# Optimization experiments

Measured on AMD Instinct MI355X. Metric: run time of the kernel, lower is better.

## Reference

```python
import jax, jax.numpy as jnp
import numpy as np
import math

N_EMBED = 2048
N_HEAD = 16
HEAD_DIM = N_EMBED // N_HEAD  # 128
ROPE_BASE = 10000.0


def _rope_tables(T, dim, dtype):
    # inv_freq over even indices, emb = concat(freqs, freqs) along last dim
    inv_freq = 1.0 / (ROPE_BASE ** (jnp.arange(0, dim, 2, dtype=jnp.float32) / dim))
    t = jnp.arange(T, dtype=jnp.float32)
    freqs = jnp.einsum('i,j->ij', t, inv_freq)          # [T, dim/2]
    emb = jnp.concatenate([freqs, freqs], axis=-1)      # [T, dim]
    return jnp.cos(emb).astype(dtype), jnp.sin(emb).astype(dtype)


def _rotate_half(x):
    h = x.shape[-1] // 2
    return jnp.concatenate([-x[..., h:], x[..., :h]], axis=-1)


def setup_inputs() -> dict:
    key = jax.random.key(0)
    ks = jax.random.split(key, 5)
    B, T, C = 32, 256, N_EMBED
    s = 1.0 / math.sqrt(C)
    return {
        'x': jax.random.normal(ks[0], (B, T, C), dtype=jnp.float32),
        'wq': jax.random.normal(ks[1], (C, C), dtype=jnp.float32) * s,
        'wk': jax.random.normal(ks[2], (C, C), dtype=jnp.float32) * s,
        'wv': jax.random.normal(ks[3], (C, C), dtype=jnp.float32) * s,
        'wo': jax.random.normal(ks[4], (C, C), dtype=jnp.float32) * s,
    }


def reference(x, wq, wk, wv, wo):
    B, T, C = x.shape
    H, D = N_HEAD, HEAD_DIM
    # torch Linear: y = x @ W^T
    q = (x @ wq.T).reshape(B, T, H, D).transpose(0, 2, 1, 3)  # [B,H,T,D]
    k = (x @ wk.T).reshape(B, T, H, D).transpose(0, 2, 1, 3)
    v = (x @ wv.T).reshape(B, T, H, D).transpose(0, 2, 1, 3)

    cos, sin = _rope_tables(T, D, x.dtype)  # [T,D] each, broadcast over B,H
    q = q * cos + _rotate_half(q) * sin
    k = k * cos + _rotate_half(k) * sin

    att = jnp.einsum('bhqd,bhkd->bhqk', q, k) / math.sqrt(D)
    causal = jnp.triu(jnp.ones((T, T), dtype=bool), k=1)
    att = jnp.where(causal, jnp.finfo(att.dtype).min, att)
    att = jax.nn.softmax(att, axis=-1)
    # dropout p=0.0 -> identity
    y = jnp.einsum('bhqk,bhkd->bhqd', att, v)
    y = y.transpose(0, 2, 1, 3).reshape(B, T, C)
    return y @ wo.T
```

## Files before the change

kernel.cpp:

```cpp
#include <hip/hip_runtime.h>

#define HB 32
#define HT 256
#define HC 2048
#define HH 16
#define HD 128
#define HM (HB * HT)

typedef __bf16 bf16x8 __attribute__((ext_vector_type(8)));
typedef float f32x4 __attribute__((ext_vector_type(4)));
typedef float f32x16 __attribute__((ext_vector_type(16)));

__device__ __forceinline__ unsigned short f2bf(float f) {
  unsigned u = __float_as_uint(f);
  u += 0x7FFFu + ((u >> 16) & 1u);
  return (unsigned short)(u >> 16);
}
__device__ __forceinline__ float bf2f(unsigned short h) {
  return __uint_as_float(((unsigned)h) << 16);
}

__global__ __launch_bounds__(256) void cvt_all(
    const float* __restrict__ x, const float* __restrict__ wq, const float* __restrict__ wk,
    const float* __restrict__ wv, const float* __restrict__ wo,
    unsigned short* __restrict__ xb, unsigned short* __restrict__ wqb,
    unsigned short* __restrict__ wkb, unsigned short* __restrict__ wvb,
    unsigned short* __restrict__ wob) {
  size_t i = (size_t)blockIdx.x * 256 + threadIdx.x;
  const float* src;
  unsigned short* dst;
  size_t off;
  if (i < 4194304) {
    src = x; dst = xb; off = i;
  } else {
    size_t j = i - 4194304;
    int w = (int)(j >> 20);
    off = j & 1048575;
    src = (w == 0) ? wq : (w == 1) ? wk : (w == 2) ? wv : wo;
    dst = (w == 0) ? wqb : (w == 1) ? wkb : (w == 2) ? wvb : wob;
  }
  float4 v = ((const float4*)src)[off];
  ushort4 o;
  o.x = f2bf(v.x); o.y = f2bf(v.y); o.z = f2bf(v.z); o.w = f2bf(v.w);
  ((ushort4*)dst)[off] = o;
}

__device__ __forceinline__ void gl_lds16(const unsigned short* g, unsigned short* l) {
  __builtin_amdgcn_global_load_lds((const __attribute__((address_space(1))) void*)g,
                                   (__attribute__((address_space(3))) void*)l, 16, 0, 0);
}

__device__ __forceinline__ void gemm_core32(const unsigned short* __restrict__ Ab,
                                            const unsigned short* __restrict__ Wb,
                                            unsigned short* lsA, unsigned short* lsB,
                                            f32x16 acc[2][2], int tid) {
  const int lane = tid & 63, wave = tid >> 6;
  const int l31 = lane & 31, half = lane >> 5;
  const int wr = wave >> 1, wc = wave & 1;
  for (int kt = 0; kt < HC / 64; ++kt) {
    __syncthreads();
#pragma unroll
    for (int i = 0; i < 4; i++) {
      int c = i * 256 + tid;
      int row = c >> 3, cc = c & 7;
      int gc = cc ^ (row & 7);
      gl_lds16(Ab + (size_t)row * HC + kt * 64 + gc * 8, lsA + c * 8);
      gl_lds16(Wb + (size_t)row * HC + kt * 64 + gc * 8, lsB + c * 8);
    }
    __syncthreads();
#pragma unroll
    for (int ks = 0; ks < 4; ++ks) {
      const int g = ks * 2 + half;
      bf16x8 af[2], bfr[2];
#pragma unroll
      for (int mi = 0; mi < 2; mi++) {
        int r = wr * 64 + mi * 32 + l31;
        int cc = g ^ (r & 7);
        af[mi] = *(const bf16x8*)(lsA + r * 64 + cc * 8);
      }
#pragma unroll
      for (int nj = 0; nj < 2; nj++) {
        int r = nj * 64 + wc * 32 + l31;
        int cc = g ^ (r & 7);
        bfr[nj] = *(const bf16x8*)(lsB + r * 64 + cc * 8);
      }
#pragma unroll
      for (int mi = 0; mi < 2; mi++)
#pragma unroll
        for (int nj = 0; nj < 2; nj++)
          acc[mi][nj] = __builtin_amdgcn_mfma_f32_32x32x16_bf16(af[mi], bfr[nj], acc[mi][nj], 0, 0, 0);
    }
  }
}

__global__ __launch_bounds__(256) void gemm_out(const unsigned short* __restrict__ A,
                                                const unsigned short* __restrict__ W,
                                                float* __restrict__ outp) {
  __shared__ __align__(16) unsigned short lsA[128 * 64];
  __shared__ __align__(16) unsigned short lsB[128 * 64];
  const int tid = threadIdx.x;
  const int lane = tid & 63, wave = tid >> 6;
  const int l31 = lane & 31, half = lane >> 5;
  const int wr = wave >> 1, wc = wave & 1;
  const int bm = blockIdx.x, bn = blockIdx.y;

  f32x16 acc[2][2];
#pragma unroll
  for (int i = 0; i < 2; i++)
#pragma unroll
    for (int j = 0; j < 2; j++)
#pragma unroll
      for (int r = 0; r < 16; r++) acc[i][j][r] = 0.f;

  gemm_core32(A + (size_t)bm * 128 * HC, W + (size_t)bn * 128 * HC, lsA, lsB, acc, tid);

#pragma unroll
  for (int mi = 0; mi < 2; mi++)
#pragma unroll
    for (int nj = 0; nj < 2; nj++)
#pragma unroll
      for (int g = 0; g < 4; g++)
#pragma unroll
        for (int rr = 0; rr < 4; rr++) {
          int m = bm * 128 + wr * 64 + mi * 32 + rr + 8 * g + 4 * half;
          int n = bn * 128 + nj * 64 + wc * 32 + l31;
          outp[(size_t)m * HC + n] = acc[mi][nj][g * 4 + rr];
        }
}

__global__ __launch_bounds__(256) void gemm_qkv(const unsigned short* __restrict__ A,
                                                const unsigned short* __restrict__ W0,
                                                const unsigned short* __restrict__ W1,
                                                const unsigned short* __restrict__ W2,
                                                unsigned short* __restrict__ Qo,
                                                unsigned short* __restrict__ Ko,
                                                unsigned short* __restrict__ Vto) {
  __shared__ __align__(16) unsigned short lsA[128 * 64];
  __shared__ __align__(16) unsigned short lsB[128 * 64];
  const int tid = threadIdx.x;
  const int lane = tid & 63, wave = tid >> 6;
  const int l31 = lane & 31, half = lane >> 5;
  const int wr = wave >> 1, wc = wave & 1;
  const int bm = blockIdx.x;
  const int which = blockIdx.y >> 4;
  const int bn = blockIdx.y & 15;

  f32x16 acc[2][2];
#pragma unroll
  for (int i = 0; i < 2; i++)
#pragma unroll
    for (int j = 0; j < 2; j++)
#pragma unroll
      for (int r = 0; r < 16; r++) acc[i][j][r] = 0.f;

  if (which < 2) {
    const unsigned short* W = (which == 0) ? W0 : W1;
    unsigned short* outp = (which == 0) ? Qo : Ko;
    gemm_core32(A + (size_t)bm * 128 * HC, W + (size_t)bn * 128 * HC, lsA, lsB, acc, tid);
    const int dlo = wc * 32 + l31;
    const float invf = __expf((float)dlo * (-0.14391156831212787f));
    const int h = bn;
#pragma unroll
    for (int mi = 0; mi < 2; mi++)
#pragma unroll
      for (int g = 0; g < 4; g++)
#pragma unroll
        for (int rr = 0; rr < 4; rr++) {
          int m = bm * 128 + wr * 64 + mi * 32 + rr + 8 * g + 4 * half;
          int t = m & 255, b = m >> 8;
          float ang = (float)t * invf;
          float sn, cs;
          __sincosf(ang, &sn, &cs);
          int reg = g * 4 + rr;
          float lo = acc[mi][0][reg], hi = acc[mi][1][reg];
          size_t base = (((size_t)b * HH + h) * HT + t) * HD;
          outp[base + dlo] = f2bf(lo * cs - hi * sn);
          outp[base + 64 + dlo] = f2bf(hi * cs + lo * sn);
        }
  } else {
    gemm_core32(W2 + (size_t)bn * 128 * HC, A + (size_t)bm * 128 * HC, lsA, lsB, acc, tid);
    const int h = bn;
#pragma unroll
    for (int mi = 0; mi < 2; mi++)
#pragma unroll
      for (int nj = 0; nj < 2; nj++)
#pragma unroll
        for (int g = 0; g < 4; g++)
#pragma unroll
          for (int rr = 0; rr < 4; rr++) {
            int d = wr * 64 + mi * 32 + rr + 8 * g + 4 * half;
            int np = bm * 128 + nj * 64 + wc * 32 + l31;
            int b = np >> 8, t = np & 255;
            Vto[(((size_t)b * HH + h) * HD + d) * HT + t] = f2bf(acc[mi][nj][g * 4 + rr]);
          }
  }
}

__global__ __launch_bounds__(256) void attn_kernel(const unsigned short* __restrict__ Q,
                                                   const unsigned short* __restrict__ K,
                                                   const unsigned short* __restrict__ Vt,
                                                   unsigned short* __restrict__ Y) {
  const int g = blockIdx.x;
  const int wq = 3 - (g >> 9);
  const int bh = g & 511;
  const int wave = threadIdx.x >> 6;
  const int lane = threadIdx.x & 63;
  const int quad = lane >> 4, l16 = lane & 15;

  const unsigned short* Qh = Q + (size_t)bh * HT * HD;
  const unsigned short* Kh = K + (size_t)bh * HT * HD;
  const unsigned short* Vh = Vt + (size_t)bh * HD * HT;

  __shared__ __align__(16) unsigned short P[4][16 * 72];
  unsigned short* Pw = P[wave];

  const int qrow = wq * 64 + wave * 16;

  bf16x8 qf[4];
#pragma unroll
  for (int ks = 0; ks < 4; ks++)
    qf[ks] = *(const bf16x8*)(Qh + (size_t)(qrow + l16) * HD + ks * 32 + quad * 8);

  f32x4 o[8];
#pragma unroll
  for (int di = 0; di < 8; di++) o[di] = f32x4{0.f, 0.f, 0.f, 0.f};
  float mrow[4], lrow[4];
#pragma unroll
  for (int r = 0; r < 4; r++) { mrow[r] = -1e30f; lrow[r] = 0.f; }

  const float scale = 0.088388347648318447f;

  for (int ct = 0; ct <= wq; ++ct) {
    f32x4 s[4];
#pragma unroll
    for (int ni = 0; ni < 4; ni++) s[ni] = f32x4{0.f, 0.f, 0.f, 0.f};
    const int nimax = (ct == wq) ? wave : 3;
#pragma unroll
    for (int ks = 0; ks < 4; ks++) {
#pragma unroll
      for (int ni = 0; ni < 4; ni++) {
        if (ni <= nimax) {
          bf16x8 kf = *(const bf16x8*)(Kh + (size_t)(ct * 64 + ni * 16 + l16) * HD + ks * 32 + quad * 8);
          s[ni] = __builtin_amdgcn_mfma_f32_16x16x32_bf16(qf[ks], kf, s[ni], 0, 0, 0);
        }
      }
    }
    if (ct == wq) {
#pragma unroll
      for (int ni = 0; ni < 4; ni++)
#pragma unroll
        for (int r = 0; r < 4; r++) {
          int qr = wave * 16 + quad * 4 + r;
          int kc = ni * 16 + l16;
          s[ni][r] = (kc <= qr) ? s[ni][r] * scale : -1e30f;
        }
    } else {
#pragma unroll
      for (int ni = 0; ni < 4; ni++)
#pragma unroll
        for (int r = 0; r < 4; r++) s[ni][r] *= scale;
    }
#pragma unroll
    for (int r = 0; r < 4; r++) {
      float v = fmaxf(fmaxf(s[0][r], s[1][r]), fmaxf(s[2][r], s[3][r]));
      v = fmaxf(v, __shfl_xor(v, 1, 64));
      v = fmaxf(v, __shfl_xor(v, 2, 64));
      v = fmaxf(v, __shfl_xor(v, 4, 64));
      v = fmaxf(v, __shfl_xor(v, 8, 64));
      float mnew = fmaxf(mrow[r], v);
      float alpha = __expf(mrow[r] - mnew);
      mrow[r] = mnew;
      float rs = 0.f;
#pragma unroll
      for (int ni = 0; ni < 4; ni++) {
        float e = __expf(s[ni][r] - mnew);
        s[ni][r] = e;
        rs += e;
      }
      rs += __shfl_xor(rs, 1, 64);
      rs += __shfl_xor(rs, 2, 64);
      rs += __shfl_xor(rs, 4, 64);
      rs += __shfl_xor(rs, 8, 64);
      lrow[r] = lrow[r] * alpha + rs;
#pragma unroll
      for (int di = 0; di < 8; di++) o[di][r] *= alpha;
    }
#pragma unroll
    for (int ni = 0; ni < 4; ni++)
#pragma unroll
      for (int r = 0; r < 4; r++)
        Pw[(quad * 4 + r) * 72 + ni * 16 + l16] = f2bf(s[ni][r]);
#pragma unroll
    for (int ks = 0; ks < 2; ks++) {
      bf16x8 pf = *(const bf16x8*)(Pw + (size_t)l16 * 72 + ks * 32 + quad * 8);
#pragma unroll
      for (int di = 0; di < 8; di++) {
        bf16x8 vf = *(const bf16x8*)(Vh + (size_t)(di * 16 + l16) * HT + ct * 64 + ks * 32 + quad * 8);
        o[di] = __builtin_amdgcn_mfma_f32_16x16x32_bf16(pf, vf, o[di], 0, 0, 0);
      }
    }
  }

  const int b = bh >> 4, h = bh & 15;
#pragma unroll
  for (int r = 0; r < 4; r++) {
    float inv = 1.f / lrow[r];
    int t = qrow + quad * 4 + r;
    size_t rowb = ((size_t)b * HT + t) * HC + h * HD;
#pragma unroll
    for (int di = 0; di < 8; di++)
      Y[rowb + di * 16 + l16] = f2bf(o[di][r] * inv);
  }
}

extern "C" void kernel_launch(void* const* d_in, const int* in_sizes, int n_in,
                              void* d_out, int out_size, void* d_ws, size_t ws_size,
                              hipStream_t stream) {
  const float* x  = (const float*)d_in[0];
  const float* wq = (const float*)d_in[1];
  const float* wk = (const float*)d_in[2];
  const float* wv = (const float*)d_in[3];
  const float* wo = (const float*)d_in[4];
  float* out = (float*)d_out;

  char* ws = (char*)d_ws;
  const size_t MB = (size_t)1 << 20;
  unsigned short* wqb = (unsigned short*)(ws + 0 * MB);
  unsigned short* wkb = (unsigned short*)(ws + 8 * MB);
  unsigned short* wvb = (unsigned short*)(ws + 16 * MB);
  unsigned short* wob = (unsigned short*)(ws + 24 * MB);
  unsigned short* xb  = (unsigned short*)(ws + 32 * MB);
  unsigned short* Qb  = (unsigned short*)(ws + 64 * MB);
  unsigned short* Kb  = (unsigned short*)(ws + 96 * MB);
  unsigned short* Vtb = (unsigned short*)(ws + 128 * MB);
  unsigned short* Yb  = xb;

  cvt_all<<<32768, 256, 0, stream>>>(x, wq, wk, wv, wo, xb, wqb, wkb, wvb, wob);

  gemm_qkv<<<dim3(HM / 128, 48), 256, 0, stream>>>(xb, wqb, wkb, wvb, Qb, Kb, Vtb);

  attn_kernel<<<2048, 256, 0, stream>>>(Qb, Kb, Vtb, Yb);

  gemm_out<<<dim3(HM / 128, HC / 128), 256, 0, stream>>>(Yb, wob, out);
}
```

Before: 545.7 us.

## Widen GEMM block tiles to 128x256 for QKV and output projections

Block tiles in both GEMMs grow from 128x128 to 128x256, so each wave now computes 2x4 MFMA 32x32 tiles instead of 2x2. The intent is to raise arithmetic intensity per LDS load and halve the number of A-tile reloads. The QKV epilogue is remapped so each wave's 128 columns form one head, which keeps RoPE pairing within a wave, and the V-transposed path swaps roles so the 256-wide side covers a full batch of tokens. This costs more accumulator registers (occupancy hinted at 2 blocks) and 48KB of LDS per block, and halves the grid size.

Result: faster. 511.3 us (-6.3%).

```diff
diff --git a/kernel.cpp b/kernel.cpp
--- a/kernel.cpp
+++ b/kernel.cpp
@@ -50,10 +50,10 @@
                                    (__attribute__((address_space(3))) void*)l, 16, 0, 0);
 }
 
-__device__ __forceinline__ void gemm_core32(const unsigned short* __restrict__ Ab,
-                                            const unsigned short* __restrict__ Wb,
-                                            unsigned short* lsA, unsigned short* lsB,
-                                            f32x16 acc[2][2], int tid) {
+__device__ __forceinline__ void gemm_core_wide(const unsigned short* __restrict__ Ab,
+                                               const unsigned short* __restrict__ Wb,
+                                               unsigned short* lsA, unsigned short* lsB,
+                                               f32x16 acc[2][4], int tid) {
   const int lane = tid & 63, wave = tid >> 6;
   const int l31 = lane & 31, half = lane >> 5;
   const int wr = wave >> 1, wc = wave & 1;
@@ -65,13 +65,19 @@
       int row = c >> 3, cc = c & 7;
       int gc = cc ^ (row & 7);
       gl_lds16(Ab + (size_t)row * HC + kt * 64 + gc * 8, lsA + c * 8);
+    }
+#pragma unroll
+    for (int i = 0; i < 8; i++) {
+      int c = i * 256 + tid;
+      int row = c >> 3, cc = c & 7;
+      int gc = cc ^ (row & 7);
       gl_lds16(Wb + (size_t)row * HC + kt * 64 + gc * 8, lsB + c * 8);
     }
     __syncthreads();
 #pragma unroll
     for (int ks = 0; ks < 4; ++ks) {
       const int g = ks * 2 + half;
-      bf16x8 af[2], bfr[2];
+      bf16x8 af[2], bfr[4];
 #pragma unroll
       for (int mi = 0; mi < 2; mi++) {
         int r = wr * 64 + mi * 32 + l31;
@@ -79,118 +85,122 @@
         af[mi] = *(const bf16x8*)(lsA + r * 64 + cc * 8);
       }
 #pragma unroll
-      for (int nj = 0; nj < 2; nj++) {
-        int r = nj * 64 + wc * 32 + l31;
+      for (int nj = 0; nj < 4; nj++) {
+        int r = wc * 128 + nj * 32 + l31;
         int cc = g ^ (r & 7);
         bfr[nj] = *(const bf16x8*)(lsB + r * 64 + cc * 8);
       }
 #pragma unroll
       for (int mi = 0; mi < 2; mi++)
 #pragma unroll
-        for (int nj = 0; nj < 2; nj++)
+        for (int nj = 0; nj < 4; nj++)
           acc[mi][nj] = __builtin_amdgcn_mfma_f32_32x32x16_bf16(af[mi], bfr[nj], acc[mi][nj], 0, 0, 0);
     }
   }
 }
 
-__global__ __launch_bounds__(256) void gemm_out(const unsigned short* __restrict__ A,
-                                                const unsigned short* __restrict__ W,
-                                                float* __restrict__ outp) {
+__global__ __launch_bounds__(256, 2) void gemm_out(const unsigned short* __restrict__ A,
+                                                   const unsigned short* __restrict__ W,
+                                                   float* __restrict__ outp) {
   __shared__ __align__(16) unsigned short lsA[128 * 64];
-  __shared__ __align__(16) unsigned short lsB[128 * 64];
+  __shared__ __align__(16) unsigned short lsB[256 * 64];
   const int tid = threadIdx.x;
   const int lane = tid & 63, wave = tid >> 6;
   const int l31 = lane & 31, half = lane >> 5;
   const int wr = wave >> 1, wc = wave & 1;
   const int bm = blockIdx.x, bn = blockIdx.y;
 
-  f32x16 acc[2][2];
+  f32x16 acc[2][4];
 #pragma unroll
   for (int i = 0; i < 2; i++)
 #pragma unroll
-    for (int j = 0; j < 2; j++)
+    for (int j = 0; j < 4; j++)
 #pragma unroll
       for (int r = 0; r < 16; r++) acc[i][j][r] = 0.f;
 
-  gemm_core32(A + (size_t)bm * 128 * HC, W + (size_t)bn * 128 * HC, lsA, lsB, acc, tid);
+  gemm_core_wide(A + (size_t)bm * 128 * HC, W + (size_t)bn * 256 * HC, lsA, lsB, acc, tid);
 
 #pragma unroll
   for (int mi = 0; mi < 2; mi++)
 #pragma unroll
-    for (int nj = 0; nj < 2; nj++)
+    for (int nj = 0; nj < 4; nj++)
 #pragma unroll
       for (int g = 0; g < 4; g++)
 #pragma unroll
         for (int rr = 0; rr < 4; rr++) {
           int m = bm * 128 + wr * 64 + mi * 32 + rr + 8 * g + 4 * half;
-          int n = bn * 128 + nj * 64 + wc * 32 + l31;
+          int n = bn * 256 + wc * 128 + nj * 32 + l31;
           outp[(size_t)m * HC + n] = acc[mi][nj][g * 4 + rr];
         }
 }
 
-__global__ __launch_bounds__(256) void gemm_qkv(const unsigned short* __restrict__ A,
-                                                const unsigned short* __restrict__ W0,
-                                                const unsigned short* __restrict__ W1,
-                                                const unsigned short* __restrict__ W2,
-                                                unsigned short* __restrict__ Qo,
-                                                unsigned short* __restrict__ Ko,
-                                                unsigned short* __restrict__ Vto) {
+__global__ __launch_bounds__(256, 2) void gemm_qkv(const unsigned short* __restrict__ A,
+                                                    const unsigned short* __restrict__ W0,
+                                                    const unsigned short* __restrict__ W1,
+                                                    const unsigned short* __restrict__ W2,
+                                                    unsigned short* __restrict__ Qo,
+                                                    unsigned short* __restrict__ Ko,
+                                                    unsigned short* __restrict__ Vto) {
   __shared__ __align__(16) unsigned short lsA[128 * 64];
-  __shared__ __align__(16) unsigned short lsB[128 * 64];
+  __shared__ __align__(16) unsigned short lsB[256 * 64];
   const int tid = threadIdx.x;
   const int lane = tid & 63, wave = tid >> 6;
   const int l31 = lane & 31, half = lane >> 5;
   const int wr = wave >> 1, wc = wave & 1;
   const int bm = blockIdx.x;
-  const int which = blockIdx.y >> 4;
-  const int bn = blockIdx.y & 15;
-
-  f32x16 acc[2][2];
+  const int which = blockIdx.y >> 3;
+  const int bn = blockIdx.y & 7;
+
+  f32x16 acc[2][4];
 #pragma unroll
   for (int i = 0; i < 2; i++)
 #pragma unroll
-    for (int j = 0; j < 2; j++)
+    for (int j = 0; j < 4; j++)
 #pragma unroll
       for (int r = 0; r < 16; r++) acc[i][j][r] = 0.f;
 
   if (which < 2) {
     const unsigned short* W = (which == 0) ? W0 : W1;
     unsigned short* outp = (which == 0) ? Qo : Ko;
-    gemm_core32(A + (size_t)bm * 128 * HC, W + (size_t)bn * 128 * HC, lsA, lsB, acc, tid);
-    const int dlo = wc * 32 + l31;
-    const float invf = __expf((float)dlo * (-0.14391156831212787f));
-    const int h = bn;
+    gemm_core_wide(A + (size_t)bm * 128 * HC, W + (size_t)bn * 256 * HC, lsA, lsB, acc, tid);
+    const int h = bn * 2 + wc;
+#pragma unroll
+    for (int nj = 0; nj < 2; nj++) {
+      const int dlo = nj * 32 + l31;
+      const float invf = __expf((float)dlo * (-0.14391156831212787f));
+#pragma unroll
+      for (int mi = 0; mi < 2; mi++)
+#pragma unroll
+        for (int g = 0; g < 4; g++)
+#pragma unroll
+          for (int rr = 0; rr < 4; rr++) {
+            int m = bm * 128 + wr * 64 + mi * 32 + rr + 8 * g + 4 * half;
+            int t = m & 255, b = m >> 8;
+            float ang = (float)t * invf;
+            float sn, cs;
+            __sincosf(ang, &sn, &cs);
+            int reg = g * 4 + rr;
+            float lo = acc[mi][nj][reg], hi = acc[mi][nj + 2][reg];
+            size_t base = (((size_t)b * HH + h) * HT + t) * HD;
+            outp[base + dlo] = f2bf(lo * cs - hi * sn);
+            outp[base + 64 + dlo] = f2bf(hi * cs + lo * sn);
+          }
+    }
+  } else {
+    int v = bn * 64 + bm;
+    int tok = v & 31, ch = v >> 5;
+    gemm_core_wide(W2 + (size_t)ch * 128 * HC, A + (size_t)tok * 256 * HC, lsA, lsB, acc, tid);
+    const int b = tok, h = ch;
 #pragma unroll
     for (int mi = 0; mi < 2; mi++)
 #pragma unroll
-      for (int g = 0; g < 4; g++)
-#pragma unroll
-        for (int rr = 0; rr < 4; rr++) {
-          int m = bm * 128 + wr * 64 + mi * 32 + rr + 8 * g + 4 * half;
-          int t = m & 255, b = m >> 8;
-          float ang = (float)t * invf;
-          float sn, cs;
-          __sincosf(ang, &sn, &cs);
-          int reg = g * 4 + rr;
-          float lo = acc[mi][0][reg], hi = acc[mi][1][reg];
-          size_t base = (((size_t)b * HH + h) * HT + t) * HD;
-          outp[base + dlo] = f2bf(lo * cs - hi * sn);
-          outp[base + 64 + dlo] = f2bf(hi * cs + lo * sn);
-        }
-  } else {
-    gemm_core32(W2 + (size_t)bn * 128 * HC, A + (size_t)bm * 128 * HC, lsA, lsB, acc, tid);
-    const int h = bn;
-#pragma unroll
-    for (int mi = 0; mi < 2; mi++)
-#pragma unroll
-      for (int nj = 0; nj < 2; nj++)
+      for (int nj = 0; nj < 4; nj++)
 #pragma unroll
         for (int g = 0; g < 4; g++)
 #pragma unroll
           for (int rr = 0; rr < 4; rr++) {
             int d = wr * 64 + mi * 32 + rr + 8 * g + 4 * half;
-            int np = bm * 128 + nj * 64 + wc * 32 + l31;
-            int b = np >> 8, t = np & 255;
+            int t = wc * 128 + nj * 32 + l31;
             Vto[(((size_t)b * HH + h) * HD + d) * HT + t] = f2bf(acc[mi][nj][g * 4 + rr]);
           }
   }
@@ -337,9 +347,9 @@
 
   cvt_all<<<32768, 256, 0, stream>>>(x, wq, wk, wv, wo, xb, wqb, wkb, wvb, wob);
 
-  gemm_qkv<<<dim3(HM / 128, 48), 256, 0, stream>>>(xb, wqb, wkb, wvb, Qb, Kb, Vtb);
+  gemm_qkv<<<dim3(HM / 128, 24), 256, 0, stream>>>(xb, wqb, wkb, wvb, Qb, Kb, Vtb);
 
   attn_kernel<<<2048, 256, 0, stream>>>(Qb, Kb, Vtb, Yb);
 
-  gemm_out<<<dim3(HM / 128, HC / 128), 256, 0, stream>>>(Yb, wob, out);
-}
+  gemm_out<<<dim3(HM / 128, HC / 256), 256, 0, stream>>>(Yb, wob, out);
+}
```
